# Kernel optimization log

Hardware: AMD Instinct MI355X
Metric: run time of the kernel (lower is better)

## Reference

```python
import jax, jax.numpy as jnp
import numpy as np

EPS = 1e-08
ITERATIONS = 3


def squash(s):
    # s: [..., d]
    s2 = jnp.sum(s * s, axis=-1, keepdims=True)
    return s2 / (1.0 + s2) * (s / jnp.sqrt(s2 + EPS))


def setup_inputs() -> dict:
    key = jax.random.key(0)
    k1, k2 = jax.random.split(key)
    B, IN_CAPS, OUT_CAPS, IN_D, OUT_D = 256, 1152, 10, 8, 16
    u = jax.random.normal(k1, (B, IN_CAPS, IN_D), dtype=jnp.float32)
    weight = jax.random.normal(k2, (IN_CAPS, OUT_CAPS, IN_D, OUT_D), dtype=jnp.float32)
    return {"u": u, "weight": weight}


def reference(u, weight):
    # u: [B, in_caps, in_d]; weight: [in_caps, out_caps, in_d, out_d]
    u_hat = jnp.einsum('ijnm,bin->bijm', weight, u)  # [B, in_caps, out_caps, out_d]
    B, in_caps, out_caps, _ = u_hat.shape
    b = jnp.zeros((B, in_caps, out_caps), dtype=u.dtype)
    v = None
    for _ in range(ITERATIONS):
        c = jax.nn.softmax(b, axis=1)  # softmax over in_caps (dim=1, faithful to source)
        s = jnp.einsum('bij,bijm->bjm', c, u_hat)  # [B, out_caps, out_d]
        v = squash(s)
        a = jnp.einsum('bjm,bijm->bij', v, u_hat)
        b = b + a
    return v
```

## Files before the change

### kernel.cpp

```cpp
#include <hip/hip_runtime.h>
#include <hip/hip_bf16.h>
#include <math.h>


#define IC 1152
#define OC 10
#define NB 256
#define TILE_DW (IC * 8)

typedef float v2f __attribute__((ext_vector_type(2)));

__device__ __forceinline__ v2f bf_v2(unsigned w) {
    v2f r = { __uint_as_float(w << 16), __uint_as_float(w & 0xFFFF0000u) };
    return r;
}
__device__ __forceinline__ unsigned pack2(float a, float b) {
    __hip_bfloat162 h = __float22bfloat162_rn(make_float2(a, b));
    return *(unsigned*)&h;
}
__device__ __forceinline__ unsigned short pack1(float a) {
    __hip_bfloat16 h = __float2bfloat16(a);
    return *(unsigned short*)&h;
}

__global__ __launch_bounds__(1024, 8)
void caps_route_kernel(const float* __restrict__ u,
                       const float* __restrict__ W,
                       float* __restrict__ out) {
    extern __shared__ unsigned smem_u[];
    unsigned* uh = smem_u;
    unsigned short* ce = (unsigned short*)(uh + 2 * TILE_DW);
    float* spart = (float*)(ce + 2 * IC);

    const int t    = threadIdx.x;
    const int bx   = blockIdx.x;
    const int lane = t & 63;
    const int wid  = t >> 6;

    int x = bx & 7, sg = bx >> 3;
    int j, p;
    if (sg < 128) { j = x; p = sg; }
    else { int s2 = sg - 128; j = 8 + (x >> 2); p = ((x & 3) << 5) + s2; }
    const int bb = p * 2;

    {
        const int q  = t & 3;
        const int i0 = t >> 2;
        const int pb = (((q >> 1) ^ ((i0 >> 2) & 1)) << 2) + ((q & 1) << 1);
        const float* u0p = u + (size_t)bb * (IC * 8);

        auto stage = [&](int i) {
            const float4* wrow = (const float4*)(W + ((size_t)(i * OC + j) << 7)) + q;
            const float4 ua0 = *(const float4*)(u0p + i * 8);
            const float4 ua1 = *(const float4*)(u0p + i * 8 + 4);
            const float4 ub0 = *(const float4*)(u0p + IC * 8 + i * 8);
            const float4 ub1 = *(const float4*)(u0p + IC * 8 + i * 8 + 4);
            v2f a01 = {0.f,0.f}, a23 = {0.f,0.f};
            v2f b01 = {0.f,0.f}, b23 = {0.f,0.f};
#define ST(ux, uy, n) {                                                   \
            const float4 w4 = wrow[(n) * 4];                              \
            const v2f w01 = {w4.x, w4.y}, w23 = {w4.z, w4.w};             \
            const v2f us = {(ux), (ux)}, vs = {(uy), (uy)};               \
            a01 += us * w01; a23 += us * w23;                             \
            b01 += vs * w01; b23 += vs * w23; }
            ST(ua0.x, ub0.x, 0) ST(ua0.y, ub0.y, 1) ST(ua0.z, ub0.z, 2) ST(ua0.w, ub0.w, 3)
            ST(ua1.x, ub1.x, 4) ST(ua1.y, ub1.y, 5) ST(ua1.z, ub1.z, 6) ST(ua1.w, ub1.w, 7)
#undef ST
            const int dst = (i << 3) + pb;
            *(uint2*)&uh[dst]           = make_uint2(pack2(a01.x, a01.y), pack2(a23.x, a23.y));
            *(uint2*)&uh[TILE_DW + dst] = make_uint2(pack2(b01.x, b01.y), pack2(b23.x, b23.y));
        };
#pragma unroll
        for (int k = 0; k < 4; ++k) stage(i0 + 256 * k);
        if (i0 < IC - 1024) stage(i0 + 1024);
    }

    __syncthreads();

    const int bt = wid >> 3;
    const int w8 = wid & 7;
    const int rowbase = w8 * 144;
    const unsigned* uhT = uh + bt * TILE_DW;
    unsigned short* ceT = ce + bt * IC;

    const int mqc = lane & 3;
    const int h   = lane >> 2;
    const int pbS = (((mqc >> 1) ^ ((h >> 2) & 1)) << 2) + ((mqc & 1) << 1);
    const bool eB = ((lane >> 2) & 1) != 0;
    const int sA0 = eB ? 2 : 0, sA1 = eB ? 3 : 1;
    const int sB0 = eB ? 0 : 2, sB1 = eB ? 1 : 3;

    float L[3];
#pragma unroll
    for (int k = 0; k < 3; ++k) L[k] = 0.f;
    float se = 0.f;
    float4 vq;

    for (int r = 0; r < 3; ++r) {
        v2f aA = {0.f, 0.f}, aB = {0.f, 0.f};
        if (r == 0) {
#pragma unroll 3
            for (int k = 0; k < 9; ++k) {
                const int i = rowbase + 16 * k + h;
                const uint2 d = *(const uint2*)&uhT[(i << 3) + pbS];
                aA += bf_v2(d.x);
                aB += bf_v2(d.y);
            }
        } else {
#pragma unroll 3
            for (int k = 0; k < 9; ++k) {
                const int i = rowbase + 16 * k + h;
                const uint2 d = *(const uint2*)&uhT[(i << 3) + pbS];
                const float c = __uint_as_float(((unsigned)ceT[i]) << 16);
                const v2f cs = {c, c};
                aA += cs * bf_v2(d.x);
                aB += cs * bf_v2(d.y);
            }
        }
        float4 acc = make_float4(aA.x, aA.y, aB.x, aB.y);
#pragma unroll
        for (int o = 4; o <= 32; o <<= 1) {
            acc.x += __shfl_xor(acc.x, o, 64); acc.y += __shfl_xor(acc.y, o, 64);
            acc.z += __shfl_xor(acc.z, o, 64); acc.w += __shfl_xor(acc.w, o, 64);
        }
        float* spR = spart + (r & 1) * 320 + bt * 160;
        if (lane < 4) *(float4*)&spR[w8 * 20 + (lane << 2)] = acc;
        else if (r > 0 && lane == 4) spR[w8 * 20 + 16] = se;
        __syncthreads();

        {
            float4 ss = {0.f, 0.f, 0.f, 0.f};
            float sesum = 0.f;
#pragma unroll
            for (int s8 = 0; s8 < 8; ++s8) {
                const float4 qq = *(const float4*)&spR[s8 * 20 + (mqc << 2)];
                ss.x += qq.x; ss.y += qq.y; ss.z += qq.z; ss.w += qq.w;
                sesum += spR[s8 * 20 + 16];
            }
            const float inv = (r == 0) ? (1.0f / (float)IC) : 1.0f / sesum;
            const float4 s4 = make_float4(ss.x * inv, ss.y * inv, ss.z * inv, ss.w * inv);
            float p2 = s4.x*s4.x + s4.y*s4.y + s4.z*s4.z + s4.w*s4.w;
            p2 += __shfl_xor(p2, 1, 64);
            p2 += __shfl_xor(p2, 2, 64);
            const float sc = p2 / ((1.0f + p2) * sqrtf(p2 + 1e-8f));
            vq = make_float4(s4.x * sc, s4.y * sc, s4.z * sc, s4.w * sc);
        }

        if (r == 2) {
            if (w8 == 0 && lane < 4)
                *(float4*)&out[((size_t)(bb + bt) * OC + j) * 16 + (lane << 2)] = vq;
        } else {
            const v2f va0 = { __shfl(vq.x, sA0, 4), __shfl(vq.y, sA0, 4) };
            const v2f va1 = { __shfl(vq.z, sA0, 4), __shfl(vq.w, sA0, 4) };
            const v2f va2 = { __shfl(vq.x, sA1, 4), __shfl(vq.y, sA1, 4) };
            const v2f va3 = { __shfl(vq.z, sA1, 4), __shfl(vq.w, sA1, 4) };
            const v2f vb0 = { __shfl(vq.x, sB0, 4), __shfl(vq.y, sB0, 4) };
            const v2f vb1 = { __shfl(vq.z, sB0, 4), __shfl(vq.w, sB0, 4) };
            const v2f vb2 = { __shfl(vq.x, sB1, 4), __shfl(vq.y, sB1, 4) };
            const v2f vb3 = { __shfl(vq.z, sB1, 4), __shfl(vq.w, sB1, 4) };
            se = 0.f;
#define BROW(i, Lk) {                                                     \
            const uint4 da = *(const uint4*)&uhT[(i) << 3];               \
            const uint4 db = *(const uint4*)&uhT[((i) << 3) + 4];         \
            v2f dp = {0.f, 0.f};                                          \
            dp += bf_v2(da.x) * va0;                                      \
            dp += bf_v2(da.y) * va1;                                      \
            dp += bf_v2(da.z) * va2;                                      \
            dp += bf_v2(da.w) * va3;                                      \
            dp += bf_v2(db.x) * vb0;                                      \
            dp += bf_v2(db.y) * vb1;                                      \
            dp += bf_v2(db.z) * vb2;                                      \
            dp += bf_v2(db.w) * vb3;                                      \
            Lk += dp.x + dp.y;                                            \
            const float ev = __expf(Lk);   \
            ceT[i] = pack1(ev);                                           \
            se += ev; }
            BROW(rowbase + lane, L[0])
            BROW(rowbase + lane + 64, L[1])
            if (lane < 16) { BROW(rowbase + 128 + lane, L[2]) }
#undef BROW
#pragma unroll
            for (int o = 32; o >= 1; o >>= 1) se += __shfl_xor(se, o, 64);
        }
    }
}

extern "C" void kernel_launch(void* const* d_in, const int* in_sizes, int n_in,
                              void* d_out, int out_size, void* d_ws, size_t ws_size,
                              hipStream_t stream) {
    const float* u = (const float*)d_in[0];
    const float* W = (const float*)d_in[1];
    float* out = (float*)d_out;

    const size_t shmem = (size_t)2 * TILE_DW * 4
                       + (size_t)2 * IC * 2
                       + 640 * 4;
    hipFuncSetAttribute((const void*)caps_route_kernel,
                        hipFuncAttributeMaxDynamicSharedMemorySize, (int)shmem);

    caps_route_kernel<<<(NB / 2) * OC, 1024, shmem, stream>>>(u, W, out);
}
```

Measured before the change: 119.2 us.

## Pre-convert W and u to fp16 and use packed fdot2 for u_hat and agreement

Adds a conversion kernel that packs W (reordered into pairs along in_d) and optionally u into fp16 in the workspace. The routing kernel then computes u_hat with v_dot2 fp16 instructions and stores u_hat in fp16 instead of bf16, and the agreement dot products also use fdot2. The aim is to halve global reads of W and cut the VALU work of the u_hat and agreement stages. In exchange it adds a separate launch and a full extra pass over W and u each call, and fp16 carries some range and precision risk.

```diff
diff --git a/kernel.cpp b/kernel.cpp
--- a/kernel.cpp
+++ b/kernel.cpp
@@ -8,14 +8,34 @@
 #define NB 256
 #define TILE_DW (IC * 8)
 
+#define NW_DW (IC * OC * 64)
+#define NU_DW (NB * IC * 4)
+#define WS_NEED ((size_t)(NW_DW + NU_DW) * 4)
+
 typedef float v2f __attribute__((ext_vector_type(2)));
-
-__device__ __forceinline__ v2f bf_v2(unsigned w) {
-    v2f r = { __uint_as_float(w << 16), __uint_as_float(w & 0xFFFF0000u) };
+typedef _Float16 h2 __attribute__((ext_vector_type(2)));
+
+#if defined(__has_builtin)
+#if __has_builtin(__builtin_amdgcn_fdot2)
+#define HAVE_FDOT2 1
+#endif
+#endif
+
+__device__ __forceinline__ float fdot2f(unsigned w, unsigned uu, float c) {
+    h2 a = *(h2*)&w, b = *(h2*)&uu;
+#ifdef HAVE_FDOT2
+    return __builtin_amdgcn_fdot2(a, b, c, false);
+#else
+    return c + (float)a.x * (float)b.x + (float)a.y * (float)b.y;
+#endif
+}
+__device__ __forceinline__ v2f h_v2(unsigned w) {
+    h2 h = *(h2*)&w;
+    v2f r = {(float)h.x, (float)h.y};
     return r;
 }
-__device__ __forceinline__ unsigned pack2(float a, float b) {
-    __hip_bfloat162 h = __float22bfloat162_rn(make_float2(a, b));
+__device__ __forceinline__ unsigned packh2(float a, float b) {
+    h2 h = {(_Float16)a, (_Float16)b};
     return *(unsigned*)&h;
 }
 __device__ __forceinline__ unsigned short pack1(float a) {
@@ -23,9 +43,30 @@
     return *(unsigned short*)&h;
 }
 
+__global__ void convert_kernel(const float* __restrict__ u,
+                               const float* __restrict__ W,
+                               unsigned* __restrict__ ws, int do_u) {
+    const int tid = blockIdx.x * blockDim.x + threadIdx.x;
+    if (tid < NW_DW) {
+        const int k = tid & 3, mp = (tid >> 2) & 3, q = (tid >> 4) & 3, ij = tid >> 6;
+        const int m = (q << 2) + mp;
+        const float* s = W + ((size_t)ij << 7) + m + (k << 5);
+        ws[tid] = packh2(s[0], s[16]);
+    } else if (do_u) {
+        const int e = tid - NW_DW;
+        if (e < NU_DW) {
+            const int pr = e & 3, bi = e >> 2;
+            const float* s = u + ((size_t)bi << 3) + (pr << 1);
+            ws[NW_DW + e] = packh2(s[0], s[1]);
+        }
+    }
+}
+
+template<bool UF16>
 __global__ __launch_bounds__(1024, 8)
 void caps_route_kernel(const float* __restrict__ u,
-                       const float* __restrict__ W,
+                       const unsigned* __restrict__ Wh,
+                       const unsigned* __restrict__ ug,
                        float* __restrict__ out) {
     extern __shared__ unsigned smem_u[];
     unsigned* uh = smem_u;
@@ -48,27 +89,40 @@
         const int i0 = t >> 2;
         const int pb = (((q >> 1) ^ ((i0 >> 2) & 1)) << 2) + ((q & 1) << 1);
         const float* u0p = u + (size_t)bb * (IC * 8);
+        const uint4* ua4 = (const uint4*)ug + (size_t)bb * IC;
+        const uint4* ub4 = ua4 + IC;
 
         auto stage = [&](int i) {
-            const float4* wrow = (const float4*)(W + ((size_t)(i * OC + j) << 7)) + q;
-            const float4 ua0 = *(const float4*)(u0p + i * 8);
-            const float4 ua1 = *(const float4*)(u0p + i * 8 + 4);
-            const float4 ub0 = *(const float4*)(u0p + IC * 8 + i * 8);
-            const float4 ub1 = *(const float4*)(u0p + IC * 8 + i * 8 + 4);
-            v2f a01 = {0.f,0.f}, a23 = {0.f,0.f};
-            v2f b01 = {0.f,0.f}, b23 = {0.f,0.f};
-#define ST(ux, uy, n) {                                                   \
-            const float4 w4 = wrow[(n) * 4];                              \
-            const v2f w01 = {w4.x, w4.y}, w23 = {w4.z, w4.w};             \
-            const v2f us = {(ux), (ux)}, vs = {(uy), (uy)};               \
-            a01 += us * w01; a23 += us * w23;                             \
-            b01 += vs * w01; b23 += vs * w23; }
-            ST(ua0.x, ub0.x, 0) ST(ua0.y, ub0.y, 1) ST(ua0.z, ub0.z, 2) ST(ua0.w, ub0.w, 3)
-            ST(ua1.x, ub1.x, 4) ST(ua1.y, ub1.y, 5) ST(ua1.z, ub1.z, 6) ST(ua1.w, ub1.w, 7)
-#undef ST
+            const uint4* wq4 = (const uint4*)Wh + (((size_t)(i * OC + j) << 2) + q) * 4;
+            uint4 Ua, Ub;
+            if constexpr (UF16) {
+                Ua = ua4[i];
+                Ub = ub4[i];
+            } else {
+                const float4 a0 = *(const float4*)(u0p + i * 8);
+                const float4 a1 = *(const float4*)(u0p + i * 8 + 4);
+                const float4 b0 = *(const float4*)(u0p + IC * 8 + i * 8);
+                const float4 b1 = *(const float4*)(u0p + IC * 8 + i * 8 + 4);
+                Ua = make_uint4(packh2(a0.x, a0.y), packh2(a0.z, a0.w),
+                                packh2(a1.x, a1.y), packh2(a1.z, a1.w));
+                Ub = make_uint4(packh2(b0.x, b0.y), packh2(b0.z, b0.w),
+                                packh2(b1.x, b1.y), packh2(b1.z, b1.w));
+            }
+            const uint4 w0 = wq4[0], w1 = wq4[1], w2 = wq4[2], w3 = wq4[3];
+            float A0, A1, A2, A3, B0, B1, B2, B3;
+#define DOT8(acc, wm) \
+            acc = fdot2f(wm.x, Ua.x, 0.f);  acc = fdot2f(wm.y, Ua.y, acc); \
+            acc = fdot2f(wm.z, Ua.z, acc);  acc = fdot2f(wm.w, Ua.w, acc);
+#define DOT8B(acc, wm) \
+            acc = fdot2f(wm.x, Ub.x, 0.f);  acc = fdot2f(wm.y, Ub.y, acc); \
+            acc = fdot2f(wm.z, Ub.z, acc);  acc = fdot2f(wm.w, Ub.w, acc);
+            DOT8(A0, w0) DOT8(A1, w1) DOT8(A2, w2) DOT8(A3, w3)
+            DOT8B(B0, w0) DOT8B(B1, w1) DOT8B(B2, w2) DOT8B(B3, w3)
+#undef DOT8
+#undef DOT8B
             const int dst = (i << 3) + pb;
-            *(uint2*)&uh[dst]           = make_uint2(pack2(a01.x, a01.y), pack2(a23.x, a23.y));
-            *(uint2*)&uh[TILE_DW + dst] = make_uint2(pack2(b01.x, b01.y), pack2(b23.x, b23.y));
+            *(uint2*)&uh[dst]           = make_uint2(packh2(A0, A1), packh2(A2, A3));
+            *(uint2*)&uh[TILE_DW + dst] = make_uint2(packh2(B0, B1), packh2(B2, B3));
         };
 #pragma unroll
         for (int k = 0; k < 4; ++k) stage(i0 + 256 * k);
@@ -103,8 +157,8 @@
             for (int k = 0; k < 9; ++k) {
                 const int i = rowbase + 16 * k + h;
                 const uint2 d = *(const uint2*)&uhT[(i << 3) + pbS];
-                aA += bf_v2(d.x);
-                aB += bf_v2(d.y);
+                aA += h_v2(d.x);
+                aB += h_v2(d.y);
             }
         } else {
 #pragma unroll 3
@@ -113,8 +167,8 @@
                 const uint2 d = *(const uint2*)&uhT[(i << 3) + pbS];
                 const float c = __uint_as_float(((unsigned)ceT[i]) << 16);
                 const v2f cs = {c, c};
-                aA += cs * bf_v2(d.x);
-                aB += cs * bf_v2(d.y);
+                aA += cs * h_v2(d.x);
+                aB += cs * h_v2(d.y);
             }
         }
         float4 acc = make_float4(aA.x, aA.y, aB.x, aB.y);
@@ -150,28 +204,24 @@
             if (w8 == 0 && lane < 4)
                 *(float4*)&out[((size_t)(bb + bt) * OC + j) * 16 + (lane << 2)] = vq;
         } else {
-            const v2f va0 = { __shfl(vq.x, sA0, 4), __shfl(vq.y, sA0, 4) };
-            const v2f va1 = { __shfl(vq.z, sA0, 4), __shfl(vq.w, sA0, 4) };
-            const v2f va2 = { __shfl(vq.x, sA1, 4), __shfl(vq.y, sA1, 4) };
-            const v2f va3 = { __shfl(vq.z, sA1, 4), __shfl(vq.w, sA1, 4) };
-            const v2f vb0 = { __shfl(vq.x, sB0, 4), __shfl(vq.y, sB0, 4) };
-            const v2f vb1 = { __shfl(vq.z, sB0, 4), __shfl(vq.w, sB0, 4) };
-            const v2f vb2 = { __shfl(vq.x, sB1, 4), __shfl(vq.y, sB1, 4) };
-            const v2f vb3 = { __shfl(vq.z, sB1, 4), __shfl(vq.w, sB1, 4) };
+            const unsigned p01 = packh2(vq.x, vq.y), p23 = packh2(vq.z, vq.w);
+            const unsigned vh0 = __shfl((int)p01, sA0, 4), vh1 = __shfl((int)p23, sA0, 4);
+            const unsigned vh2 = __shfl((int)p01, sA1, 4), vh3 = __shfl((int)p23, sA1, 4);
+            const unsigned vh4 = __shfl((int)p01, sB0, 4), vh5 = __shfl((int)p23, sB0, 4);
+            const unsigned vh6 = __shfl((int)p01, sB1, 4), vh7 = __shfl((int)p23, sB1, 4);
             se = 0.f;
 #define BROW(i, Lk) {                                                     \
             const uint4 da = *(const uint4*)&uhT[(i) << 3];               \
             const uint4 db = *(const uint4*)&uhT[((i) << 3) + 4];         \
-            v2f dp = {0.f, 0.f};                                          \
-            dp += bf_v2(da.x) * va0;                                      \
-            dp += bf_v2(da.y) * va1;                                      \
-            dp += bf_v2(da.z) * va2;                                      \
-            dp += bf_v2(da.w) * va3;                                      \
-            dp += bf_v2(db.x) * vb0;                                      \
-            dp += bf_v2(db.y) * vb1;                                      \
-            dp += bf_v2(db.z) * vb2;                                      \
-            dp += bf_v2(db.w) * vb3;                                      \
-            Lk += dp.x + dp.y;                                            \
+            float dpA = fdot2f(da.x, vh0, 0.f);                           \
+            dpA = fdot2f(da.y, vh1, dpA);                                 \
+            dpA = fdot2f(da.z, vh2, dpA);                                 \
+            dpA = fdot2f(da.w, vh3, dpA);                                 \
+            float dpB = fdot2f(db.x, vh4, 0.f);                           \
+            dpB = fdot2f(db.y, vh5, dpB);                                 \
+            dpB = fdot2f(db.z, vh6, dpB);                                 \
+            dpB = fdot2f(db.w, vh7, dpB);                                 \
+            Lk += dpA + dpB;                                              \
             const float ev = __expf(Lk);   \
             ceT[i] = pack1(ev);                                           \
             se += ev; }
@@ -191,12 +241,22 @@
     const float* u = (const float*)d_in[0];
     const float* W = (const float*)d_in[1];
     float* out = (float*)d_out;
+    unsigned* ws = (unsigned*)d_ws;
+
+    const int do_u = (ws_size >= WS_NEED) ? 1 : 0;
+    const int total = NW_DW + (do_u ? NU_DW : 0);
+    convert_kernel<<<(total + 255) / 256, 256, 0, stream>>>(u, W, ws, do_u);
 
     const size_t shmem = (size_t)2 * TILE_DW * 4
                        + (size_t)2 * IC * 2
                        + 640 * 4;
-    hipFuncSetAttribute((const void*)caps_route_kernel,
-                        hipFuncAttributeMaxDynamicSharedMemorySize, (int)shmem);
-
-    caps_route_kernel<<<(NB / 2) * OC, 1024, shmem, stream>>>(u, W, out);
-}
+    if (do_u) {
+        hipFuncSetAttribute((const void*)caps_route_kernel<true>,
+                            hipFuncAttributeMaxDynamicSharedMemorySize, (int)shmem);
+        caps_route_kernel<true><<<(NB / 2) * OC, 1024, shmem, stream>>>(u, ws, ws + NW_DW, out);
+    } else {
+        hipFuncSetAttribute((const void*)caps_route_kernel<false>,
+                            hipFuncAttributeMaxDynamicSharedMemorySize, (int)shmem);
+        caps_route_kernel<false><<<(NB / 2) * OC, 1024, shmem, stream>>>(u, ws, ws + NW_DW, out);
+    }
+}
```

New measurement: 112.4 us. 5.8% less time.
